# Kernel optimization log

Measured on AMD Instinct MI355X. Metric: run time of the kernel, lower is better.

The kernel has to match this reference:

```python
import jax, jax.numpy as jnp
import numpy as np

BN_EPS = 1e-5


def setup_inputs() -> dict:
    key = jax.random.key(0)
    ks = jax.random.split(key, 5)
    b, c, h, w = 4, 256, 64, 64
    pre = jax.random.normal(ks[0], (b, c, h, w), dtype=jnp.float32)
    cur = jax.random.normal(ks[1], (b, c, h, w), dtype=jnp.float32)
    # 1x1 conv weight stored as [out_ch, in_ch] (kernel is 1x1)
    W = jax.random.normal(ks[2], (256, 2 * c), dtype=jnp.float32) * (1.0 / np.sqrt(2 * c))
    b_conv = jax.random.normal(ks[3], (256,), dtype=jnp.float32) * 0.01
    gamma = jnp.ones((256,), dtype=jnp.float32)
    beta = jnp.zeros((256,), dtype=jnp.float32)
    run_mean = jnp.zeros((256,), dtype=jnp.float32)
    run_var = jnp.ones((256,), dtype=jnp.float32)
    alpha = jnp.full((1,), 0.25, dtype=jnp.float32)  # PReLU single shared slope
    return {"pre": pre, "cur": cur, "W": W, "b_conv": b_conv, "gamma": gamma,
            "beta": beta, "run_mean": run_mean, "run_var": run_var, "alpha": alpha}


def reference(pre, cur, W, b_conv, gamma, beta, run_mean, run_var, alpha):
    b, c, h, w = cur.shape
    hw = h * w
    pre_a = pre.reshape(b, c, hw)            # [b, c, hw]
    cur_a = cur.reshape(b, c, hw)            # [b, c, hw]
    # scores[b, i, j] = sum_c pre[b,c,i] * cur[b,c,j]
    scores = jnp.einsum('bci,bcj->bij', pre_a, cur_a)
    attn = jax.nn.softmax(scores * (c ** -0.5), axis=-1)   # [b, hw, hw]
    # feat[b, c, i] = sum_j attn[b,i,j] * cur[b,c,j]
    feat = jnp.einsum('bij,bcj->bci', attn, cur_a)          # [b, c, hw]
    x = jnp.concatenate([feat, cur_a], axis=1).reshape(b, 2 * c, h, w)
    # 1x1 conv
    y = jnp.einsum('bchw,oc->bohw', x, W) + b_conv[None, :, None, None]
    # BatchNorm2d (inference: running stats)
    inv = gamma * jax.lax.rsqrt(run_var + BN_EPS)
    y = y * inv[None, :, None, None] + (beta - run_mean * inv)[None, :, None, None]
    # PReLU (single shared parameter)
    a = alpha[0]
    return jnp.where(y >= 0, y, a * y)
```

## Files before the change

kernel.cpp:

```cpp
#include <hip/hip_runtime.h>
#include <hip/hip_bf16.h>
#include <math.h>

#define HWX 4096
#define CCH 256
#define NB  4

typedef __attribute__((ext_vector_type(8))) short short8;
typedef __attribute__((ext_vector_type(4))) short short4v;
typedef __attribute__((ext_vector_type(4))) float f32x4;
typedef __attribute__((ext_vector_type(2))) float f32x2;

#define WS_QT 0ull
#define WS_KT 8388608ull
#define WS_V  16777216ull
#define WS_W  25165824ull
#define WS_FT 25427968ull
#define WS_PO 33816576ull

__device__ __forceinline__ short f2bf(float f) {
  union { float f; unsigned u; } a; a.f = f;
  unsigned r = a.u + 0x7FFFu + ((a.u >> 16) & 1u);
  return (short)(r >> 16);
}

__device__ __forceinline__ float bf2f(short s) {
  union { unsigned u; float f; } a;
  a.u = ((unsigned)(unsigned short)s) << 16;
  return a.f;
}

__device__ __forceinline__ short f2bf_rn(float f) {
  __hip_bfloat16 h = __float2bfloat16(f);
  return *reinterpret_cast<short*>(&h);
}

__device__ __forceinline__ f32x4 mfma16(short8 a, short8 b, f32x4 c) {
  return __builtin_amdgcn_mfma_f32_16x16x32_bf16(a, b, c, 0, 0, 0);
}

__device__ __forceinline__ void gload16(const void* g, void* l) {
  __builtin_amdgcn_global_load_lds(
      (const __attribute__((address_space(1))) unsigned int*)g,
      (__attribute__((address_space(3))) unsigned int*)l, 16, 0, 0);
}

__device__ __forceinline__ int kt_invmap(int j) {
  return (((j >> 2) & 1) << 4) | (((j >> 3) & 3) << 2) | (j & 3);
}

__global__ __launch_bounds__(256) void prep_qkv(const float* __restrict__ pre,
                                                const float* __restrict__ cur,
                                                char* __restrict__ ws) {
  __shared__ short ldsT[256 * 36];
  const int tid = threadIdx.x;
  const int b  = blockIdx.x >> 7;
  const int jt = blockIdx.x & 127;
  const int j0 = jt * 32;
  const float* preB = pre + (size_t)b * CCH * HWX + j0;
  const float* curB = cur + (size_t)b * CCH * HWX + j0;
  char* vout = ws + WS_V  + (size_t)(b * 128 + jt) * 16384;
  char* kout = ws + WS_KT + (size_t)(b * 128 + jt) * 16384;
  char* qout = ws + WS_QT + (size_t)(b * 128 + jt) * 16384;

  short v[32];
  {
    const float* p = curB + (size_t)tid * HWX;
#pragma unroll
    for (int k = 0; k < 8; ++k) {
      f32x4 f = *(const f32x4*)(p + k * 4);
      v[k*4+0] = f2bf(f[0]); v[k*4+1] = f2bf(f[1]);
      v[k*4+2] = f2bf(f[2]); v[k*4+3] = f2bf(f[3]);
    }
  }
#pragma unroll
  for (int k = 0; k < 4; ++k) {
    short8 o8;
#pragma unroll
    for (int e = 0; e < 8; ++e) o8[e] = v[k * 8 + e];
    *(short8*)(vout + ((tid * 64 + k * 16) ^ ((tid & 7) << 4))) = o8;
  }
#pragma unroll
  for (int j = 0; j < 32; ++j) ldsT[tid * 36 + j] = v[j];
  __syncthreads();
  {
    const int j = tid >> 3, m = tid & 7;
    const int a = kt_invmap(j);
#pragma unroll
    for (int k = 0; k < 4; ++k) {
      short8 o8;
#pragma unroll
      for (int e = 0; e < 8; ++e) o8[e] = ldsT[(m * 32 + k * 8 + e) * 36 + j];
      *(short8*)(kout + ((a * 512 + m * 64 + k * 16) ^ ((a & 7) << 4))) = o8;
    }
  }
  __syncthreads();
  {
    const float* p = preB + (size_t)tid * HWX;
#pragma unroll
    for (int k = 0; k < 8; ++k) {
      f32x4 f = *(const f32x4*)(p + k * 4);
      v[k*4+0] = f2bf(f[0]); v[k*4+1] = f2bf(f[1]);
      v[k*4+2] = f2bf(f[2]); v[k*4+3] = f2bf(f[3]);
    }
  }
#pragma unroll
  for (int j = 0; j < 32; ++j) ldsT[tid * 36 + j] = v[j];
  __syncthreads();
  {
    const int j = tid >> 3, m = tid & 7;
#pragma unroll
    for (int k = 0; k < 4; ++k) {
      short8 o8;
#pragma unroll
      for (int e = 0; e < 8; ++e) o8[e] = ldsT[(m * 32 + k * 8 + e) * 36 + j];
      *(short8*)(qout + ((j * 512 + m * 64 + k * 16) ^ ((j & 7) << 4))) = o8;
    }
  }
}

__global__ __launch_bounds__(256) void prep_w(const float* __restrict__ Wm,
                                              char* __restrict__ ws) {
  const int sl = blockIdx.x;
  const int o  = threadIdx.x;
  char* out = ws + WS_W + (size_t)sl * 32768;
  const float* src = Wm + (size_t)o * 512 + sl * 64;
  short tmp[64];
#pragma unroll
  for (int k = 0; k < 16; ++k) {
    f32x4 f = *(const f32x4*)(src + k * 4);
    tmp[k*4+0] = f2bf(f[0]); tmp[k*4+1] = f2bf(f[1]);
    tmp[k*4+2] = f2bf(f[2]); tmp[k*4+3] = f2bf(f[3]);
  }
#pragma unroll
  for (int k = 0; k < 8; ++k) {
    short8 o8;
#pragma unroll
    for (int e = 0; e < 8; ++e) o8[e] = tmp[k * 8 + e];
    *(short8*)(out + ((o * 128 + k * 16) ^ ((o & 7) << 4))) = o8;
  }
}

__global__ __launch_bounds__(256, 2) void attn_db4(char* __restrict__ ws) {
  __shared__ __align__(16) char smem[65536];
  const int tid = threadIdx.x, lane = tid & 63, wv = tid >> 6;
  const int g = lane >> 4, l15 = lane & 15;
  const int p = blockIdx.x;
  const int L = (p & 7) * 64 + (p >> 3);
  const int b = L >> 7, s = (L >> 5) & 3, it = L & 31;
  const int i0 = it * 128;
  const int NT = 32;
  const char* qimg  = ws + WS_QT + (size_t)(b * 128 + it * 4) * 16384;
  const char* kbase = ws + WS_KT + (size_t)(b * 128 + s * NT) * 16384;
  const char* vbase = ws + WS_V  + (size_t)(b * 128 + s * NT) * 16384;

#pragma unroll
  for (int k = 0; k < 16; ++k)
    gload16(qimg + k * 4096 + tid * 16, smem + k * 4096 + tid * 16);
  __syncthreads();
  short8 qf[2][8];
  {
    const char* qt = smem + wv * 16384;
#pragma unroll
    for (int qsub = 0; qsub < 2; ++qsub)
#pragma unroll
      for (int kb = 0; kb < 8; ++kb)
        qf[qsub][kb] = *(const short8*)(qt + (qsub * 16 + l15) * 512 +
                                        ((kb * 64 + g * 16) ^ ((l15 & 7) << 4)));
  }
  __syncthreads();

  f32x4 acc[2][16];
#pragma unroll
  for (int qsub = 0; qsub < 2; ++qsub)
#pragma unroll
    for (int nt = 0; nt < 16; ++nt) acc[qsub][nt] = (f32x4){0.f, 0.f, 0.f, 0.f};
  f32x4 accl[2];
  accl[0] = (f32x4){0.f, 0.f, 0.f, 0.f};
  accl[1] = (f32x4){0.f, 0.f, 0.f, 0.f};
  const float SL2E = 1.4426950408889634f / 16.0f;
  short8 ones;
#pragma unroll
  for (int e = 0; e < 8; ++e) ones[e] = (short)16256;

#pragma unroll
  for (int k = 0; k < 4; ++k) {
    gload16(kbase + k * 4096 + tid * 16, smem + k * 4096 + tid * 16);
    gload16(vbase + k * 4096 + tid * 16, smem + 16384 + k * 4096 + tid * 16);
  }
  __syncthreads();

  int cur = 0;
  for (int t = 0; t < NT; ++t) {
    if (t + 1 < NT) {
      const char* ks = kbase + (size_t)(t + 1) * 16384;
      const char* vs = vbase + (size_t)(t + 1) * 16384;
      char* dst = smem + (cur ^ 1) * 32768 + tid * 16;
#pragma unroll
      for (int k = 0; k < 4; ++k) {
        gload16(ks + k * 4096 + tid * 16, dst + k * 4096);
        gload16(vs + k * 4096 + tid * 16, dst + 16384 + k * 4096);
      }
    }
    const char* bk = smem + cur * 32768;
    const char* bv = bk + 16384;
    f32x4 s00 = (f32x4){0.f,0.f,0.f,0.f}, s01 = (f32x4){0.f,0.f,0.f,0.f};
    f32x4 s10 = (f32x4){0.f,0.f,0.f,0.f}, s11 = (f32x4){0.f,0.f,0.f,0.f};
    __builtin_amdgcn_s_setprio(1);
#pragma unroll
    for (int kb = 0; kb < 8; ++kb) {
      const int co = (kb * 64 + g * 16) ^ ((l15 & 7) << 4);
      short8 k0 = *(const short8*)(bk + l15 * 512 + co);
      short8 k1 = *(const short8*)(bk + (l15 + 16) * 512 + co);
      s00 = mfma16(k0, qf[0][kb], s00);
      s01 = mfma16(k1, qf[0][kb], s01);
      s10 = mfma16(k0, qf[1][kb], s10);
      s11 = mfma16(k1, qf[1][kb], s11);
    }
    __builtin_amdgcn_s_setprio(0);
    short8 pf0, pf1;
#pragma unroll
    for (int r = 0; r < 4; ++r) {
      pf0[r]     = f2bf_rn(exp2f(fmaf(s00[r], SL2E, -16.0f)));
      pf0[4 + r] = f2bf_rn(exp2f(fmaf(s01[r], SL2E, -16.0f)));
      pf1[r]     = f2bf_rn(exp2f(fmaf(s10[r], SL2E, -16.0f)));
      pf1[4 + r] = f2bf_rn(exp2f(fmaf(s11[r], SL2E, -16.0f)));
    }
    __builtin_amdgcn_s_setprio(1);
    accl[0] = mfma16(pf0, ones, accl[0]);
    accl[1] = mfma16(pf1, ones, accl[1]);
#pragma unroll
    for (int nt = 0; nt < 16; ++nt) {
      const int c = nt * 16 + l15;
      short8 vf = *(const short8*)(bv + ((c * 64 + g * 16) ^ ((c & 7) << 4)));
      acc[0][nt] = mfma16(pf0, vf, acc[0][nt]);
      acc[1][nt] = mfma16(pf1, vf, acc[1][nt]);
    }
    __builtin_amdgcn_s_setprio(0);
    __syncthreads();
    cur ^= 1;
  }

  short* po = (short*)(ws + WS_PO) + (size_t)(s * NB + b) * CCH * HWX;
#pragma unroll
  for (int qsub = 0; qsub < 2; ++qsub)
#pragma unroll
    for (int nt = 0; nt < 16; ++nt) {
      const int c = nt * 16 + l15;
      short4v o4;
#pragma unroll
      for (int r = 0; r < 4; ++r) o4[r] = f2bf_rn(acc[qsub][nt][r]);
      *(short4v*)(po + (size_t)c * HWX + i0 + wv * 32 + qsub * 16 + g * 4) = o4;
    }
  if (l15 == 0) {
    short* pl = (short*)(ws + WS_PO + 4ull * 8388608ull) +
                (size_t)(s * NB + b) * HWX + i0 + wv * 32 + g * 4;
    short4v a4, b4;
#pragma unroll
    for (int r = 0; r < 4; ++r) { a4[r] = f2bf_rn(accl[0][r]); b4[r] = f2bf_rn(accl[1][r]); }
    *(short4v*)pl = a4;
    *(short4v*)(pl + 16) = b4;
  }
}

template <int S>
__global__ __launch_bounds__(128, 2) void attn_sb(char* __restrict__ ws) {
  __shared__ __align__(16) char smem[32768];
  const int tid = threadIdx.x, lane = tid & 63, wv = tid >> 6;
  const int g = lane >> 4, l15 = lane & 15;
  const int p = blockIdx.x;
  const int NT = 128 / S;
  int b, s, it;
  if (S == 2) {
    const int L = (p & 7) * 64 + (p >> 3);
    b = L >> 7; s = (L >> 6) & 1; it = L & 63;
  } else {
    const int L = (p & 7) * 32 + (p >> 3);
    b = L >> 6; s = 0; it = L & 63;
  }
  const int i0 = it * 64;
  const char* qimg  = ws + WS_QT + (size_t)(b * 128 + it * 2) * 16384;
  const char* kbase = ws + WS_KT + (size_t)(b * 128 + s * NT) * 16384;
  const char* vbase = ws + WS_V  + (size_t)(b * 128 + s * NT) * 16384;

#pragma unroll
  for (int k = 0; k < 16; ++k)
    gload16(qimg + k * 2048 + tid * 16, smem + k * 2048 + tid * 16);
  __syncthreads();
  short8 qf[2][8];
  {
    const char* qt = smem + wv * 16384;
#pragma unroll
    for (int qsub = 0; qsub < 2; ++qsub)
#pragma unroll
      for (int kb = 0; kb < 8; ++kb)
        qf[qsub][kb] = *(const short8*)(qt + (qsub * 16 + l15) * 512 +
                                        ((kb * 64 + g * 16) ^ ((l15 & 7) << 4)));
  }
  __syncthreads();

  f32x4 acc[2][16];
#pragma unroll
  for (int qsub = 0; qsub < 2; ++qsub)
#pragma unroll
    for (int nt = 0; nt < 16; ++nt) acc[qsub][nt] = (f32x4){0.f, 0.f, 0.f, 0.f};
  f32x4 accl[2];
  accl[0] = (f32x4){0.f, 0.f, 0.f, 0.f};
  accl[1] = (f32x4){0.f, 0.f, 0.f, 0.f};
  const float SL2E = 1.4426950408889634f / 16.0f;
  short8 ones;
#pragma unroll
  for (int e = 0; e < 8; ++e) ones[e] = (short)16256;

#pragma unroll
  for (int k = 0; k < 8; ++k) {
    gload16(kbase + k * 2048 + tid * 16, smem + k * 2048 + tid * 16);
    gload16(vbase + k * 2048 + tid * 16, smem + 16384 + k * 2048 + tid * 16);
  }
  __syncthreads();

  for (int t = 0; t < NT; ++t) {
    const char* bk = smem;
    const char* bv = smem + 16384;
    f32x4 s00 = (f32x4){0.f,0.f,0.f,0.f}, s01 = (f32x4){0.f,0.f,0.f,0.f};
    f32x4 s10 = (f32x4){0.f,0.f,0.f,0.f}, s11 = (f32x4){0.f,0.f,0.f,0.f};
    __builtin_amdgcn_s_setprio(1);
#pragma unroll
    for (int kb = 0; kb < 8; ++kb) {
      const int co = (kb * 64 + g * 16) ^ ((l15 & 7) << 4);
      short8 k0 = *(const short8*)(bk + l15 * 512 + co);
      short8 k1 = *(const short8*)(bk + (l15 + 16) * 512 + co);
      s00 = mfma16(k0, qf[0][kb], s00);
      s01 = mfma16(k1, qf[0][kb], s01);
      s10 = mfma16(k0, qf[1][kb], s10);
      s11 = mfma16(k1, qf[1][kb], s11);
    }
    __builtin_amdgcn_s_setprio(0);
    short8 pf0, pf1;
#pragma unroll
    for (int r = 0; r < 4; ++r) {
      pf0[r]     = f2bf_rn(exp2f(fmaf(s00[r], SL2E, -16.0f)));
      pf0[4 + r] = f2bf_rn(exp2f(fmaf(s01[r], SL2E, -16.0f)));
      pf1[r]     = f2bf_rn(exp2f(fmaf(s10[r], SL2E, -16.0f)));
      pf1[4 + r] = f2bf_rn(exp2f(fmaf(s11[r], SL2E, -16.0f)));
    }
    __builtin_amdgcn_s_setprio(1);
    accl[0] = mfma16(pf0, ones, accl[0]);
    accl[1] = mfma16(pf1, ones, accl[1]);
#pragma unroll
    for (int nt = 0; nt < 16; ++nt) {
      const int c = nt * 16 + l15;
      short8 vf = *(const short8*)(bv + ((c * 64 + g * 16) ^ ((c & 7) << 4)));
      acc[0][nt] = mfma16(pf0, vf, acc[0][nt]);
      acc[1][nt] = mfma16(pf1, vf, acc[1][nt]);
    }
    __builtin_amdgcn_s_setprio(0);
    __syncthreads();
    if (t + 1 < NT) {
      const char* ks = kbase + (size_t)(t + 1) * 16384;
      const char* vs = vbase + (size_t)(t + 1) * 16384;
#pragma unroll
      for (int k = 0; k < 8; ++k) {
        gload16(ks + k * 2048 + tid * 16, smem + k * 2048 + tid * 16);
        gload16(vs + k * 2048 + tid * 16, smem + 16384 + k * 2048 + tid * 16);
      }
    }
    __syncthreads();
  }

  short* po = (short*)(ws + WS_PO) + (size_t)(s * NB + b) * CCH * HWX;
#pragma unroll
  for (int qsub = 0; qsub < 2; ++qsub)
#pragma unroll
    for (int nt = 0; nt < 16; ++nt) {
      const int c = nt * 16 + l15;
      short4v o4;
#pragma unroll
      for (int r = 0; r < 4; ++r) o4[r] = f2bf_rn(acc[qsub][nt][r]);
      *(short4v*)(po + (size_t)c * HWX + i0 + wv * 32 + qsub * 16 + g * 4) = o4;
    }
  if (l15 == 0) {
    short* pl = (short*)(ws + WS_PO + (size_t)S * 8388608ull) +
                (size_t)(s * NB + b) * HWX + i0 + wv * 32 + g * 4;
    short4v a4, b4;
#pragma unroll
    for (int r = 0; r < 4; ++r) { a4[r] = f2bf_rn(accl[0][r]); b4[r] = f2bf_rn(accl[1][r]); }
    *(short4v*)pl = a4;
    *(short4v*)(pl + 16) = b4;
  }
}

template <int S>
__global__ __launch_bounds__(256) void merge_feat(char* __restrict__ ws) {
  __shared__ float linv[32];
  __shared__ short ldsT[32 * 66];
  const int tid = threadIdx.x;
  const int p = blockIdx.x;
  const int L = (p & 7) * 64 + (p >> 3);
  const int b = L >> 7, it = L & 127, i0 = it * 32;
  const short* po = (const short*)(ws + WS_PO);
  const short* pl = (const short*)(ws + WS_PO + (size_t)S * 8388608ull);
  if (tid < 32) {
    float l = 0.0f;
#pragma unroll
    for (int s = 0; s < S; ++s)
      l += bf2f(pl[(size_t)(s * NB + b) * HWX + i0 + tid]);
    linv[tid] = 1.0f / l;
  }
  __syncthreads();
  char* fout = ws + WS_FT + (size_t)(b * 128 + it) * 16384;
#pragma unroll
  for (int ch = 0; ch < 4; ++ch) {
    const int c = ch * 64 + (tid >> 2);
    const int qo = (tid & 3) * 8;
    float a[8];
#pragma unroll
    for (int e = 0; e < 8; ++e) a[e] = 0.0f;
#pragma unroll
    for (int s = 0; s < S; ++s) {
      short8 v8 = *(const short8*)(po + (size_t)(s * NB + b) * CCH * HWX +
                                   (size_t)c * HWX + i0 + qo);
#pragma unroll
      for (int e = 0; e < 8; ++e) a[e] += bf2f(v8[e]);
    }
#pragma unroll
    for (int e = 0; e < 8; ++e)
      ldsT[(qo + e) * 66 + (tid >> 2)] = f2bf(a[e] * linv[qo + e]);
    __syncthreads();
    {
      const int i = tid >> 3, m = tid & 7;
      short8 o8;
#pragma unroll
      for (int e = 0; e < 8; ++e) o8[e] = ldsT[i * 66 + m * 8 + e];
      *(short8*)(fout + ((i * 512 + ch * 128 + m * 16) ^ ((i & 7) << 4))) = o8;
    }
    __syncthreads();
  }
}

__global__ __launch_bounds__(256) void conv_mfma(const float* __restrict__ bconv,
                                                 const float* __restrict__ gamma,
                                                 const float* __restrict__ beta,
                                                 const float* __restrict__ rmean,
                                                 const float* __restrict__ rvar,
                                                 const float* __restrict__ alpha,
                                                 char* __restrict__ ws,
                                                 float* __restrict__ out) {
  __shared__ __align__(16) char smem[73728];
  const int tid = threadIdx.x, lane = tid & 63, wv = tid >> 6;
  const int g = lane >> 4, l15 = lane & 15;
  const int p = blockIdx.x;
  const int L = (p & 7) * 64 + (p >> 3);
  const int b = L >> 7, it = L & 127, i0 = it * 32;
  const char* wimg = ws + WS_W;
  const char* ft = ws + WS_FT + (size_t)(b * 128 + it) * 16384;
  const char* kt = ws + WS_KT + (size_t)(b * 128 + it) * 16384;

  f32x4 acc[4][2];
#pragma unroll
  for (int ot = 0; ot < 4; ++ot)
#pragma unroll
    for (int itt = 0; itt < 2; ++itt) acc[ot][itt] = (f32x4){0.f, 0.f, 0.f, 0.f};

  const int xi = wv * 8 + (lane >> 3), xw = (lane & 7) * 16;

#pragma unroll
  for (int k = 0; k < 8; ++k)
    gload16(wimg + wv * 8192 + k * 1024 + lane * 16,
            smem + wv * 8192 + k * 1024 + lane * 16);
  gload16(ft + xi * 512 + xw, smem + 65536 + wv * 1024 + lane * 16);
  __syncthreads();

  int cur = 0;
  for (int st = 0; st < 8; ++st) {
    if (st < 7) {
      const int sn = st + 1;
      const char* img = (sn < 4) ? ft : kt;
      const int coff = (sn & 3) * 128;
#pragma unroll
      for (int k = 0; k < 8; ++k)
        gload16(wimg + (size_t)sn * 32768 + wv * 8192 + k * 1024 + lane * 16,
                smem + (cur ^ 1) * 32768 + wv * 8192 + k * 1024 + lane * 16);
      gload16(img + xi * 512 + coff + xw,
              smem + 65536 + (cur ^ 1) * 4096 + wv * 1024 + lane * 16);
    }
    const char* wb = smem + cur * 32768;
    const char* xb = smem + 65536 + cur * 4096;
    short8 bx[2][2];
#pragma unroll
    for (int itt = 0; itt < 2; ++itt) {
      const int i = itt * 16 + l15;
      const int ii = (st < 4) ? i : kt_invmap(i);
#pragma unroll
      for (int kb = 0; kb < 2; ++kb)
        bx[itt][kb] = *(const short8*)(xb + ii * 128 + ((kb * 64 + g * 16) ^ ((ii & 7) << 4)));
    }
#pragma unroll
    for (int ot = 0; ot < 4; ++ot) {
      const int o = wv * 64 + ot * 16 + l15;
#pragma unroll
      for (int kb = 0; kb < 2; ++kb) {
        short8 aw = *(const short8*)(wb + o * 128 + ((kb * 64 + g * 16) ^ ((o & 7) << 4)));
#pragma unroll
        for (int itt = 0; itt < 2; ++itt)
          acc[ot][itt] = mfma16(aw, bx[itt][kb], acc[ot][itt]);
      }
    }
    __syncthreads();
    cur ^= 1;
  }

  const float a0 = alpha[0];
  float* outB = out + (size_t)b * CCH * HWX;
#pragma unroll
  for (int ot = 0; ot < 4; ++ot)
#pragma unroll
    for (int r = 0; r < 4; ++r) {
      const int o = wv * 64 + ot * 16 + g * 4 + r;
      const float inv = gamma[o] * rsqrtf(rvar[o] + 1e-5f);
      const float add = beta[o] - rmean[o] * inv + bconv[o] * inv;
#pragma unroll
      for (int itt = 0; itt < 2; ++itt) {
        float v = acc[ot][itt][r] * inv + add;
        v = (v >= 0.0f) ? v : a0 * v;
        outB[(size_t)o * HWX + i0 + itt * 16 + l15] = v;
      }
    }
}

__global__ __launch_bounds__(256) void legacy_attn(const float* __restrict__ pre,
                                                   const float* __restrict__ cur,
                                                   float* __restrict__ feat) {
  __shared__ __align__(16) char smem[43008];
  short* lds_q  = (short*)smem;
  short* lds_kT = (short*)smem;
  short* lds_v  = (short*)(smem + 16896);
  short* lds_p  = (short*)(smem + 37376);
  const int tid = threadIdx.x, lane = tid & 63, wv = tid >> 6;
  const int b = blockIdx.x >> 6, i0 = (blockIdx.x & 63) * 64;
  const float* preB = pre + (size_t)b * CCH * HWX;
  const float* curB = cur + (size_t)b * CCH * HWX;
  float* featB = feat + (size_t)b * CCH * HWX;
  {
    const int ib = (tid & 15) * 4, cbb = (tid >> 4) * 4;
#pragma unroll
    for (int p = 0; p < 4; ++p) {
      const int c = cbb + 64 * p;
      f32x4 f[4];
#pragma unroll
      for (int r = 0; r < 4; ++r)
        f[r] = *(const f32x4*)(preB + (size_t)(c + r) * HWX + i0 + ib);
#pragma unroll
      for (int e = 0; e < 4; ++e) {
        short4v s2;
        s2[0] = f2bf(f[0][e]); s2[1] = f2bf(f[1][e]);
        s2[2] = f2bf(f[2][e]); s2[3] = f2bf(f[3][e]);
        *(short4v*)(&lds_q[(ib + e) * 264 + c]) = s2;
      }
    }
  }
  __syncthreads();
  short8 qf[8];
  {
    const int r = wv * 16 + (lane & 15), ko = (lane >> 4) * 8;
#pragma unroll
    for (int kb = 0; kb < 8; ++kb)
      qf[kb] = *(const short8*)(&lds_q[r * 264 + kb * 32 + ko]);
  }
  f32x4 acc[16];
#pragma unroll
  for (int nt = 0; nt < 16; ++nt) acc[nt] = (f32x4){0.f, 0.f, 0.f, 0.f};
  float m_run[4], l_run[4];
#pragma unroll
  for (int r = 0; r < 4; ++r) { m_run[r] = -1e30f; l_run[r] = 0.0f; }
  const float SL2E = 1.4426950408889634f / 16.0f;
  for (int jt = 0; jt < 128; ++jt) {
    const int j0 = jt * 32;
    __syncthreads();
    {
      const int jb = (tid & 7) * 4, cbb = (tid >> 3) * 4;
#pragma unroll
      for (int p = 0; p < 2; ++p) {
        const int c = cbb + 128 * p;
        f32x4 f[4];
#pragma unroll
        for (int r = 0; r < 4; ++r)
          f[r] = *(const f32x4*)(curB + (size_t)(c + r) * HWX + j0 + jb);
#pragma unroll
        for (int r = 0; r < 4; ++r) {
          short4v s2;
          s2[0] = f2bf(f[r][0]); s2[1] = f2bf(f[r][1]);
          s2[2] = f2bf(f[r][2]); s2[3] = f2bf(f[r][3]);
          *(short4v*)(&lds_v[(c + r) * 40 + jb]) = s2;
        }
#pragma unroll
        for (int e = 0; e < 4; ++e) {
          short4v s2;
          s2[0] = f2bf(f[0][e]); s2[1] = f2bf(f[1][e]);
          s2[2] = f2bf(f[2][e]); s2[3] = f2bf(f[3][e]);
          *(short4v*)(&lds_kT[(jb + e) * 264 + c]) = s2;
        }
      }
    }
    __syncthreads();
    f32x4 s0 = (f32x4){0.f,0.f,0.f,0.f}, s1 = (f32x4){0.f,0.f,0.f,0.f};
    {
      const int jc = lane & 15, ko = (lane >> 4) * 8;
#pragma unroll
      for (int kb = 0; kb < 8; ++kb) {
        short8 k0 = *(const short8*)(&lds_kT[jc * 264 + kb * 32 + ko]);
        short8 k1 = *(const short8*)(&lds_kT[(jc + 16) * 264 + kb * 32 + ko]);
        s0 = mfma16(qf[kb], k0, s0);
        s1 = mfma16(qf[kb], k1, s1);
      }
    }
    float p0[4], p1[4], corr[4];
#pragma unroll
    for (int r = 0; r < 4; ++r) {
      float t = fmaxf(s0[r], s1[r]);
      t = fmaxf(t, __shfl_xor(t, 1)); t = fmaxf(t, __shfl_xor(t, 2));
      t = fmaxf(t, __shfl_xor(t, 4)); t = fmaxf(t, __shfl_xor(t, 8));
      const float mn = fmaxf(m_run[r], t * SL2E);
      corr[r] = exp2f(m_run[r] - mn);
      m_run[r] = mn;
      p0[r] = exp2f(s0[r] * SL2E - mn);
      p1[r] = exp2f(s1[r] * SL2E - mn);
      float rs = p0[r] + p1[r];
      rs += __shfl_xor(rs, 1); rs += __shfl_xor(rs, 2);
      rs += __shfl_xor(rs, 4); rs += __shfl_xor(rs, 8);
      l_run[r] = l_run[r] * corr[r] + rs;
    }
#pragma unroll
    for (int nt = 0; nt < 16; ++nt)
#pragma unroll
      for (int r = 0; r < 4; ++r) acc[nt][r] *= corr[r];
    {
      short* pw = lds_p + wv * 640;
      const int g2 = lane >> 4, jc = lane & 15;
#pragma unroll
      for (int r = 0; r < 4; ++r) {
        pw[(g2 * 4 + r) * 40 + jc]      = f2bf(p0[r]);
        pw[(g2 * 4 + r) * 40 + 16 + jc] = f2bf(p1[r]);
      }
    }
    {
      const int g2 = lane >> 4, rr = lane & 15;
      short8 pf = *(const short8*)(&lds_p[wv * 640 + rr * 40 + g2 * 8]);
#pragma unroll
      for (int nt = 0; nt < 16; ++nt) {
        short8 vf = *(const short8*)(&lds_v[(nt * 16 + rr) * 40 + g2 * 8]);
        acc[nt] = mfma16(pf, vf, acc[nt]);
      }
    }
  }
  {
    const int g2 = lane >> 4, jc = lane & 15;
    float rl[4];
#pragma unroll
    for (int r = 0; r < 4; ++r) rl[r] = 1.0f / l_run[r];
#pragma unroll
    for (int nt = 0; nt < 16; ++nt) {
      const int c = nt * 16 + jc;
#pragma unroll
      for (int r = 0; r < 4; ++r)
        featB[(size_t)c * HWX + i0 + wv * 16 + g2 * 4 + r] = acc[nt][r] * rl[r];
    }
  }
}

__global__ __launch_bounds__(256) void legacy_conv(const float* feat,
                                                   const float* __restrict__ cur,
                                                   const float* __restrict__ Wm,
                                                   const float* __restrict__ bconv,
                                                   const float* __restrict__ gamma,
                                                   const float* __restrict__ beta,
                                                   const float* __restrict__ rmean,
                                                   const float* __restrict__ rvar,
                                                   const float* __restrict__ alpha,
                                                   float* out) {
  __shared__ __align__(16) char smem[25600];
  short* lds_w = (short*)smem;
  short* lds_x = (short*)(smem + 20480);
  const int tid = threadIdx.x, lane = tid & 63, wv = tid >> 6;
  const int b = blockIdx.x >> 6, i0 = (blockIdx.x & 63) * 64;
  const float* featB = feat + (size_t)b * CCH * HWX;
  const float* curB  = cur  + (size_t)b * CCH * HWX;
  f32x4 acc[4][4];
#pragma unroll
  for (int ot = 0; ot < 4; ++ot)
#pragma unroll
    for (int it = 0; it < 4; ++it) acc[ot][it] = (f32x4){0.f, 0.f, 0.f, 0.f};
  for (int ks = 0; ks < 16; ++ks) {
    const int k0 = ks * 32;
    __syncthreads();
    {
      const int kq = (tid & 7) * 4, ob = tid >> 3;
#pragma unroll
      for (int p = 0; p < 8; ++p) {
        const int o = ob + 32 * p;
        f32x4 f = *(const f32x4*)(Wm + (size_t)o * 512 + k0 + kq);
        short4v s2;
        s2[0] = f2bf(f[0]); s2[1] = f2bf(f[1]); s2[2] = f2bf(f[2]); s2[3] = f2bf(f[3]);
        *(short4v*)(&lds_w[o * 40 + kq]) = s2;
      }
    }
    {
      const int i2 = (tid & 31) * 2, cc = ((tid >> 5) & 7) * 4;
      const float* basep = (k0 < 256) ? (featB + (size_t)(k0 + cc) * HWX)
                                      : (curB + (size_t)(k0 + cc - 256) * HWX);
      f32x2 f[4];
#pragma unroll
      for (int r = 0; r < 4; ++r)
        f[r] = *(const f32x2*)(basep + (size_t)r * HWX + i0 + i2);
#pragma unroll
      for (int e = 0; e < 2; ++e) {
        short4v s2;
        s2[0] = f2bf(f[0][e]); s2[1] = f2bf(f[1][e]);
        s2[2] = f2bf(f[2][e]); s2[3] = f2bf(f[3][e]);
        *(short4v*)(&lds_x[(i2 + e) * 40 + cc]) = s2;
      }
    }
    __syncthreads();
    {
      const int g = lane >> 4, rr = lane & 15;
      short8 af[4], bx[4];
#pragma unroll
      for (int ot = 0; ot < 4; ++ot)
        af[ot] = *(const short8*)(&lds_w[(wv * 64 + ot * 16 + rr) * 40 + g * 8]);
#pragma unroll
      for (int it = 0; it < 4; ++it)
        bx[it] = *(const short8*)(&lds_x[(it * 16 + rr) * 40 + g * 8]);
#pragma unroll
      for (int ot = 0; ot < 4; ++ot)
#pragma unroll
        for (int it = 0; it < 4; ++it)
          acc[ot][it] = mfma16(af[ot], bx[it], acc[ot][it]);
    }
  }
  const float a0 = alpha[0];
  const int g = lane >> 4, ic = lane & 15;
  float* outB = out + (size_t)b * CCH * HWX;
#pragma unroll
  for (int ot = 0; ot < 4; ++ot)
#pragma unroll
    for (int r = 0; r < 4; ++r) {
      const int o = wv * 64 + ot * 16 + g * 4 + r;
      const float inv = gamma[o] * rsqrtf(rvar[o] + 1e-5f);
      const float add = beta[o] - rmean[o] * inv + bconv[o] * inv;
#pragma unroll
      for (int it = 0; it < 4; ++it) {
        float v = acc[ot][it][r] * inv + add;
        v = (v >= 0.0f) ? v : a0 * v;
        outB[(size_t)o * HWX + i0 + it * 16 + ic] = v;
      }
    }
}

extern "C" void kernel_launch(void* const* d_in, const int* in_sizes, int n_in,
                              void* d_out, int out_size, void* d_ws, size_t ws_size,
                              hipStream_t stream) {
  (void)in_sizes; (void)n_in; (void)out_size;
  const float* pre   = (const float*)d_in[0];
  const float* cur   = (const float*)d_in[1];
  const float* Wm    = (const float*)d_in[2];
  const float* bconv = (const float*)d_in[3];
  const float* gamma = (const float*)d_in[4];
  const float* beta  = (const float*)d_in[5];
  const float* rmean = (const float*)d_in[6];
  const float* rvar  = (const float*)d_in[7];
  const float* alpha = (const float*)d_in[8];
  float* out = (float*)d_out;
  char* ws = (char*)d_ws;

  const size_t need4 = WS_PO + 4ull * (8388608ull + 32768ull);
  const size_t need2 = WS_PO + 2ull * (8388608ull + 32768ull);
  const size_t need1 = WS_PO + 1ull * (8388608ull + 32768ull);

  if (ws_size >= need1) {
    prep_qkv<<<dim3(512), dim3(256), 0, stream>>>(pre, cur, ws);
    prep_w<<<dim3(8), dim3(256), 0, stream>>>(Wm, ws);
    if (ws_size >= need4) {
      attn_db4<<<dim3(512), dim3(256), 0, stream>>>(ws);
      merge_feat<4><<<dim3(512), dim3(256), 0, stream>>>(ws);
    } else if (ws_size >= need2) {
      attn_sb<2><<<dim3(512), dim3(128), 0, stream>>>(ws);
      merge_feat<2><<<dim3(512), dim3(256), 0, stream>>>(ws);
    } else {
      attn_sb<1><<<dim3(256), dim3(128), 0, stream>>>(ws);
      merge_feat<1><<<dim3(512), dim3(256), 0, stream>>>(ws);
    }
    conv_mfma<<<dim3(512), dim3(256), 0, stream>>>(bconv, gamma, beta, rmean,
                                                   rvar, alpha, ws, out);
  } else {
    legacy_attn<<<dim3(256), dim3(256), 0, stream>>>(pre, cur, out);
    legacy_conv<<<dim3(256), dim3(256), 0, stream>>>(out, cur, Wm, bconv, gamma,
                                                     beta, rmean, rvar, alpha, out);
  }
}
```

Baseline: 124.6 us.

## Software-pipeline QK scores one tile ahead of PV in attention kernel

Restructures the main attention loop so that the QK^T scores and exp of tile t+1 are computed while the PV MFMAs consume the probabilities of tile t. The K and V buffers are split into separately double-buffered regions, with K prefetched two tiles ahead before compute and V prefetched after the barrier. The aim is to overlap the exp/convert VALU work and the LDS reads with matrix-core work and to hide load latency better. It also swaps the library bf16 round-to-nearest conversion for a cheaper custom bit-trick version everywhere, which can treat NaN differently.

```diff
diff --git a/kernel.cpp b/kernel.cpp
--- a/kernel.cpp
+++ b/kernel.cpp
@@ -28,11 +28,6 @@
   union { unsigned u; float f; } a;
   a.u = ((unsigned)(unsigned short)s) << 16;
   return a.f;
-}
-
-__device__ __forceinline__ short f2bf_rn(float f) {
-  __hip_bfloat16 h = __float2bfloat16(f);
-  return *reinterpret_cast<short*>(&h);
 }
 
 __device__ __forceinline__ f32x4 mfma16(short8 a, short8 b, f32x4 c) {
@@ -141,7 +136,7 @@
   }
 }
 
-__global__ __launch_bounds__(256, 2) void attn_db4(char* __restrict__ ws) {
+__global__ __launch_bounds__(256, 2) void attn_pipe(char* __restrict__ ws) {
   __shared__ __align__(16) char smem[65536];
   const int tid = threadIdx.x, lane = tid & 63, wv = tid >> 6;
   const int g = lane >> 4, l15 = lane & 15;
@@ -185,60 +180,96 @@
 
 #pragma unroll
   for (int k = 0; k < 4; ++k) {
-    gload16(kbase + k * 4096 + tid * 16, smem + k * 4096 + tid * 16);
-    gload16(vbase + k * 4096 + tid * 16, smem + 16384 + k * 4096 + tid * 16);
-  }
-  __syncthreads();
-
-  int cur = 0;
-  for (int t = 0; t < NT; ++t) {
-    if (t + 1 < NT) {
-      const char* ks = kbase + (size_t)(t + 1) * 16384;
-      const char* vs = vbase + (size_t)(t + 1) * 16384;
-      char* dst = smem + (cur ^ 1) * 32768 + tid * 16;
-#pragma unroll
-      for (int k = 0; k < 4; ++k) {
-        gload16(ks + k * 4096 + tid * 16, dst + k * 4096);
-        gload16(vs + k * 4096 + tid * 16, dst + 16384 + k * 4096);
-      }
-    }
-    const char* bk = smem + cur * 32768;
-    const char* bv = bk + 16384;
+    gload16(kbase +         k * 4096 + tid * 16, smem +         k * 4096 + tid * 16);
+    gload16(kbase + 16384 + k * 4096 + tid * 16, smem + 16384 + k * 4096 + tid * 16);
+    gload16(vbase +         k * 4096 + tid * 16, smem + 32768 + k * 4096 + tid * 16);
+    gload16(vbase + 16384 + k * 4096 + tid * 16, smem + 49152 + k * 4096 + tid * 16);
+  }
+  __syncthreads();
+
+  short8 pfA0, pfA1, pfB0, pfB1;
+#pragma unroll
+  for (int e = 0; e < 8; ++e) { pfB0[e] = 0; pfB1[e] = 0; }
+  {
     f32x4 s00 = (f32x4){0.f,0.f,0.f,0.f}, s01 = (f32x4){0.f,0.f,0.f,0.f};
     f32x4 s10 = (f32x4){0.f,0.f,0.f,0.f}, s11 = (f32x4){0.f,0.f,0.f,0.f};
-    __builtin_amdgcn_s_setprio(1);
 #pragma unroll
     for (int kb = 0; kb < 8; ++kb) {
       const int co = (kb * 64 + g * 16) ^ ((l15 & 7) << 4);
-      short8 k0 = *(const short8*)(bk + l15 * 512 + co);
-      short8 k1 = *(const short8*)(bk + (l15 + 16) * 512 + co);
+      short8 k0 = *(const short8*)(smem + l15 * 512 + co);
+      short8 k1 = *(const short8*)(smem + (l15 + 16) * 512 + co);
       s00 = mfma16(k0, qf[0][kb], s00);
       s01 = mfma16(k1, qf[0][kb], s01);
       s10 = mfma16(k0, qf[1][kb], s10);
       s11 = mfma16(k1, qf[1][kb], s11);
     }
-    __builtin_amdgcn_s_setprio(0);
-    short8 pf0, pf1;
 #pragma unroll
     for (int r = 0; r < 4; ++r) {
-      pf0[r]     = f2bf_rn(exp2f(fmaf(s00[r], SL2E, -16.0f)));
-      pf0[4 + r] = f2bf_rn(exp2f(fmaf(s01[r], SL2E, -16.0f)));
-      pf1[r]     = f2bf_rn(exp2f(fmaf(s10[r], SL2E, -16.0f)));
-      pf1[4 + r] = f2bf_rn(exp2f(fmaf(s11[r], SL2E, -16.0f)));
+      pfA0[r]     = f2bf(exp2f(fmaf(s00[r], SL2E, -16.0f)));
+      pfA0[4 + r] = f2bf(exp2f(fmaf(s01[r], SL2E, -16.0f)));
+      pfA1[r]     = f2bf(exp2f(fmaf(s10[r], SL2E, -16.0f)));
+      pfA1[4 + r] = f2bf(exp2f(fmaf(s11[r], SL2E, -16.0f)));
+    }
+  }
+  __syncthreads();
+
+  auto body = [&](int tc, char* kpd, const char* kqk, const char* vpv,
+                  char* vpd, short8& pi0, short8& pi1,
+                  short8& po0, short8& po1) {
+    if (tc + 2 < NT) {
+      const char* ks = kbase + (size_t)(tc + 2) * 16384;
+#pragma unroll
+      for (int k = 0; k < 4; ++k)
+        gload16(ks + k * 4096 + tid * 16, kpd + k * 4096 + tid * 16);
+    }
+    if (tc + 1 < NT) {
+      f32x4 s00 = (f32x4){0.f,0.f,0.f,0.f}, s01 = (f32x4){0.f,0.f,0.f,0.f};
+      f32x4 s10 = (f32x4){0.f,0.f,0.f,0.f}, s11 = (f32x4){0.f,0.f,0.f,0.f};
+      __builtin_amdgcn_s_setprio(1);
+#pragma unroll
+      for (int kb = 0; kb < 8; ++kb) {
+        const int co = (kb * 64 + g * 16) ^ ((l15 & 7) << 4);
+        short8 k0 = *(const short8*)(kqk + l15 * 512 + co);
+        short8 k1 = *(const short8*)(kqk + (l15 + 16) * 512 + co);
+        s00 = mfma16(k0, qf[0][kb], s00);
+        s01 = mfma16(k1, qf[0][kb], s01);
+        s10 = mfma16(k0, qf[1][kb], s10);
+        s11 = mfma16(k1, qf[1][kb], s11);
+      }
+      __builtin_amdgcn_s_setprio(0);
+#pragma unroll
+      for (int r = 0; r < 4; ++r) {
+        po0[r]     = f2bf(exp2f(fmaf(s00[r], SL2E, -16.0f)));
+        po0[4 + r] = f2bf(exp2f(fmaf(s01[r], SL2E, -16.0f)));
+        po1[r]     = f2bf(exp2f(fmaf(s10[r], SL2E, -16.0f)));
+        po1[4 + r] = f2bf(exp2f(fmaf(s11[r], SL2E, -16.0f)));
+      }
     }
     __builtin_amdgcn_s_setprio(1);
-    accl[0] = mfma16(pf0, ones, accl[0]);
-    accl[1] = mfma16(pf1, ones, accl[1]);
+    accl[0] = mfma16(pi0, ones, accl[0]);
+    accl[1] = mfma16(pi1, ones, accl[1]);
 #pragma unroll
     for (int nt = 0; nt < 16; ++nt) {
       const int c = nt * 16 + l15;
-      short8 vf = *(const short8*)(bv + ((c * 64 + g * 16) ^ ((c & 7) << 4)));
-      acc[0][nt] = mfma16(pf0, vf, acc[0][nt]);
-      acc[1][nt] = mfma16(pf1, vf, acc[1][nt]);
+      short8 vf = *(const short8*)(vpv + ((c * 64 + g * 16) ^ ((c & 7) << 4)));
+      acc[0][nt] = mfma16(pi0, vf, acc[0][nt]);
+      acc[1][nt] = mfma16(pi1, vf, acc[1][nt]);
     }
     __builtin_amdgcn_s_setprio(0);
     __syncthreads();
-    cur ^= 1;
+    if (tc + 2 < NT) {
+      const char* vs = vbase + (size_t)(tc + 2) * 16384;
+#pragma unroll
+      for (int k = 0; k < 4; ++k)
+        gload16(vs + k * 4096 + tid * 16, vpd + k * 4096 + tid * 16);
+    }
+  };
+
+  for (int t = 0; t < NT; t += 2) {
+    body(t,     smem,         smem + 16384, smem + 32768, smem + 32768,
+         pfA0, pfA1, pfB0, pfB1);
+    body(t + 1, smem + 16384, smem,         smem + 49152, smem + 49152,
+         pfB0, pfB1, pfA0, pfA1);
   }
 
   short* po = (short*)(ws + WS_PO) + (size_t)(s * NB + b) * CCH * HWX;
@@ -249,7 +280,7 @@
       const int c = nt * 16 + l15;
       short4v o4;
 #pragma unroll
-      for (int r = 0; r < 4; ++r) o4[r] = f2bf_rn(acc[qsub][nt][r]);
+      for (int r = 0; r < 4; ++r) o4[r] = f2bf(acc[qsub][nt][r]);
       *(short4v*)(po + (size_t)c * HWX + i0 + wv * 32 + qsub * 16 + g * 4) = o4;
     }
   if (l15 == 0) {
@@ -257,7 +288,7 @@
                 (size_t)(s * NB + b) * HWX + i0 + wv * 32 + g * 4;
     short4v a4, b4;
 #pragma unroll
-    for (int r = 0; r < 4; ++r) { a4[r] = f2bf_rn(accl[0][r]); b4[r] = f2bf_rn(accl[1][r]); }
+    for (int r = 0; r < 4; ++r) { a4[r] = f2bf(accl[0][r]); b4[r] = f2bf(accl[1][r]); }
     *(short4v*)pl = a4;
     *(short4v*)(pl + 16) = b4;
   }
@@ -339,10 +370,10 @@
     short8 pf0, pf1;
 #pragma unroll
     for (int r = 0; r < 4; ++r) {
-      pf0[r]     = f2bf_rn(exp2f(fmaf(s00[r], SL2E, -16.0f)));
-      pf0[4 + r] = f2bf_rn(exp2f(fmaf(s01[r], SL2E, -16.0f)));
-      pf1[r]     = f2bf_rn(exp2f(fmaf(s10[r], SL2E, -16.0f)));
-      pf1[4 + r] = f2bf_rn(exp2f(fmaf(s11[r], SL2E, -16.0f)));
+      pf0[r]     = f2bf(exp2f(fmaf(s00[r], SL2E, -16.0f)));
+      pf0[4 + r] = f2bf(exp2f(fmaf(s01[r], SL2E, -16.0f)));
+      pf1[r]     = f2bf(exp2f(fmaf(s10[r], SL2E, -16.0f)));
+      pf1[4 + r] = f2bf(exp2f(fmaf(s11[r], SL2E, -16.0f)));
     }
     __builtin_amdgcn_s_setprio(1);
     accl[0] = mfma16(pf0, ones, accl[0]);
@@ -376,7 +407,7 @@
       const int c = nt * 16 + l15;
       short4v o4;
 #pragma unroll
-      for (int r = 0; r < 4; ++r) o4[r] = f2bf_rn(acc[qsub][nt][r]);
+      for (int r = 0; r < 4; ++r) o4[r] = f2bf(acc[qsub][nt][r]);
       *(short4v*)(po + (size_t)c * HWX + i0 + wv * 32 + qsub * 16 + g * 4) = o4;
     }
   if (l15 == 0) {
@@ -384,7 +415,7 @@
                 (size_t)(s * NB + b) * HWX + i0 + wv * 32 + g * 4;
     short4v a4, b4;
 #pragma unroll
-    for (int r = 0; r < 4; ++r) { a4[r] = f2bf_rn(accl[0][r]); b4[r] = f2bf_rn(accl[1][r]); }
+    for (int r = 0; r < 4; ++r) { a4[r] = f2bf(accl[0][r]); b4[r] = f2bf(accl[1][r]); }
     *(short4v*)pl = a4;
     *(short4v*)(pl + 16) = b4;
   }
@@ -780,7 +811,7 @@
     prep_qkv<<<dim3(512), dim3(256), 0, stream>>>(pre, cur, ws);
     prep_w<<<dim3(8), dim3(256), 0, stream>>>(Wm, ws);
     if (ws_size >= need4) {
-      attn_db4<<<dim3(512), dim3(256), 0, stream>>>(ws);
+      attn_pipe<<<dim3(512), dim3(256), 0, stream>>>(ws);
       merge_feat<4><<<dim3(512), dim3(256), 0, stream>>>(ws);
     } else if (ws_size >= need2) {
       attn_sb<2><<<dim3(512), dim3(128), 0, stream>>>(ws);
```

New measurement: 160.9 us. +29.2%, slower.
